# Optimization experiments

Hardware: AMD Instinct MI355X
Metric: run time of the kernel (lower is better)

The kernel has to match this reference:

```python
import jax, jax.numpy as jnp
import numpy as np

NEG_SLOPE = 0.01  # torch nn.LeakyReLU default


def setup_inputs() -> dict:
    key = jax.random.key(0)
    k1, k2, k3, k4 = jax.random.split(key, 4)
    B, N, d = 256, 64, 64
    embeddings = jax.random.normal(k1, (B, N, d), dtype=jnp.float32)
    # nn.Linear(em_dim, em_dim): weight [d, d] (out, in), bias [d]
    w_W = jax.random.normal(k2, (d, d), dtype=jnp.float32) / np.sqrt(d)
    w_b = jax.random.normal(k3, (d,), dtype=jnp.float32) * 0.01
    # nn.Linear(em_dim, 1): weight [1, d] -> stored as [d], bias [1]
    a_W = jax.random.normal(k4, (d,), dtype=jnp.float32) / np.sqrt(d)
    a_b = jnp.zeros((1,), dtype=jnp.float32)
    return {"embeddings": embeddings, "w_W": w_W, "w_b": w_b, "a_W": a_W, "a_b": a_b}


def reference(embeddings, w_W, w_b, a_W, a_b):
    # pairwise elementwise product: value[b,i,j,d] = emb[b,i,d] * emb[b,j,d]
    value = embeddings[:, :, None, :] * embeddings[:, None, :, :]  # [B,N,N,d]
    # small linear d->d (torch Linear: x @ W.T + b)
    qk = jnp.einsum('bijd,ed->bije', value, w_W) + w_b
    qk = jnp.where(qk >= 0, qk, NEG_SLOPE * qk)  # LeakyReLU
    # dropout is identity in eval mode
    logits = jnp.einsum('bijd,d->bij', qk, a_W) + a_b[0]  # linear d->1, squeeze
    alphas = jax.nn.softmax(logits, axis=-1)[..., None]  # [B,N,N,1]
    return alphas, value
```

## Files before the change

### kernel.cpp

```cpp
#include <hip/hip_runtime.h>

typedef __attribute__((ext_vector_type(8))) short short8;
typedef __attribute__((ext_vector_type(4))) float floatx4;

#define NEG_SLOPE 0.01f

__device__ __forceinline__ unsigned bfr(float f) {
    unsigned u = __float_as_uint(f);
    return (u + 0x7FFFu + ((u >> 16) & 1u)) >> 16;
}
__device__ __forceinline__ int pack2(float x, float y) {
    return (int)bfr(x) | (int)(bfr(y) << 16);
}
__device__ __forceinline__ short8 packfrag(float4 a, float4 b) {
    union { int i[4]; short8 s; } u;
    u.i[0] = pack2(a.x, a.y); u.i[1] = pack2(a.z, a.w);
    u.i[2] = pack2(b.x, b.y); u.i[3] = pack2(b.z, b.w);
    return u.s;
}

__global__ __launch_bounds__(256, 4)
void afm_kernel(const float* __restrict__ emb,
                const float* __restrict__ wW,
                const float* __restrict__ wb,
                const float* __restrict__ aW,
                float* __restrict__ aOut,
                float* __restrict__ vOut) {
    __shared__ float slog[4][64];

    const int tid  = threadIdx.x;
    const int lane = tid & 63;
    const int w    = tid >> 6;
    const int lo   = lane & 15;
    const int hi   = lane >> 4;
    const int blk  = blockIdx.x;
    const int b    = blk >> 4;
    const int i    = ((blk & 15) << 2) + w;

    const float* embB   = emb + ((size_t)b << 12);
    const float* ei_row = embB + (i << 6);

    {
        float4 ei = *(const float4*)(ei_row + (lo << 2));
        float* base = vOut + (((size_t)((b << 6) + i)) << 12) + (lane << 2);
        #pragma unroll
        for (int c = 0; c < 16; ++c) {
            float4 ej = *(const float4*)(embB + ((((c << 2) + hi)) << 6) + (lo << 2));
            floatx4 v;
            v[0] = ei.x * ej.x; v[1] = ei.y * ej.y;
            v[2] = ei.z * ej.z; v[3] = ei.w * ej.w;
            __builtin_nontemporal_store(v, (floatx4*)(base + (c << 8)));
        }
    }

    floatx4 acc[4][4];
    #pragma unroll
    for (int jt = 0; jt < 4; ++jt)
        #pragma unroll
        for (int et = 0; et < 4; ++et)
            acc[jt][et] = (floatx4){0.f, 0.f, 0.f, 0.f};

    #pragma unroll
    for (int kt = 0; kt < 2; ++kt) {
        const int d0 = (kt << 5) + (hi << 3);
        float4 ei0 = *(const float4*)(ei_row + d0);
        float4 ei1 = *(const float4*)(ei_row + d0 + 4);
        short8 bfrag[4];
        #pragma unroll
        for (int et = 0; et < 4; ++et) {
            const float* pw = wW + ((((et << 4) + lo)) << 6) + d0;
            float4 w0 = *(const float4*)(pw);
            float4 w1 = *(const float4*)(pw + 4);
            float4 p0, p1;
            p0.x = w0.x * ei0.x; p0.y = w0.y * ei0.y;
            p0.z = w0.z * ei0.z; p0.w = w0.w * ei0.w;
            p1.x = w1.x * ei1.x; p1.y = w1.y * ei1.y;
            p1.z = w1.z * ei1.z; p1.w = w1.w * ei1.w;
            bfrag[et] = packfrag(p0, p1);
        }
        #pragma unroll
        for (int jt = 0; jt < 4; ++jt) {
            const float* pe = embB + ((((jt << 4) + lo)) << 6) + d0;
            float4 a0 = *(const float4*)(pe);
            float4 a1 = *(const float4*)(pe + 4);
            short8 afrag = packfrag(a0, a1);
            #pragma unroll
            for (int et = 0; et < 4; ++et)
                acc[jt][et] = __builtin_amdgcn_mfma_f32_16x16x32_bf16(
                    afrag, bfrag[et], acc[jt][et], 0, 0, 0);
        }
    }

    float wbv[4], awv[4];
    #pragma unroll
    for (int et = 0; et < 4; ++et) {
        wbv[et] = wb[(et << 4) + lo];
        awv[et] = aW[(et << 4) + lo];
    }

    float lg[16];
    #pragma unroll
    for (int jt = 0; jt < 4; ++jt) {
        #pragma unroll
        for (int r = 0; r < 4; ++r) {
            float p = 0.f;
            #pragma unroll
            for (int et = 0; et < 4; ++et) {
                float x = acc[jt][et][r] + wbv[et];
                x = (x >= 0.f) ? x : NEG_SLOPE * x;
                p += awv[et] * x;
            }
            p += __shfl_xor(p, 1);
            p += __shfl_xor(p, 2);
            p += __shfl_xor(p, 4);
            p += __shfl_xor(p, 8);
            lg[jt * 4 + r] = p;
        }
    }

    float m = lg[0];
    #pragma unroll
    for (int k = 1; k < 16; ++k) m = fmaxf(m, lg[k]);
    m = fmaxf(m, __shfl_xor(m, 16));
    m = fmaxf(m, __shfl_xor(m, 32));

    float ex[16];
    float s = 0.f;
    #pragma unroll
    for (int k = 0; k < 16; ++k) { ex[k] = __expf(lg[k] - m); s += ex[k]; }
    s += __shfl_xor(s, 16);
    s += __shfl_xor(s, 32);
    float inv = 1.f / s;

    if (lo == 0) {
        #pragma unroll
        for (int jt = 0; jt < 4; ++jt)
            #pragma unroll
            for (int r = 0; r < 4; ++r)
                slog[w][jt * 16 + hi * 4 + r] = ex[jt * 4 + r] * inv;
    }
    asm volatile("" ::: "memory");
    aOut[(((size_t)((b << 6) + i)) << 6) + lane] = slog[w][lane];
}

extern "C" void kernel_launch(void* const* d_in, const int* in_sizes, int n_in,
                              void* d_out, int out_size, void* d_ws, size_t ws_size,
                              hipStream_t stream) {
    const float* emb = (const float*)d_in[0];
    const float* wW  = (const float*)d_in[1];
    const float* wb  = (const float*)d_in[2];
    const float* aW  = (const float*)d_in[3];
    float* aOut = (float*)d_out;
    float* vOut = aOut + (size_t)256 * 64 * 64;
    afm_kernel<<<4096, 256, 0, stream>>>(emb, wW, wb, aW, aOut, vOut);
}
```

Baseline: 329.8 us.

## Stage batch embeddings in LDS as fp32 and bf16, hoist weight fragments

Each block now loads the 64x64 embedding tile of its batch into shared memory once, keeping an fp32 copy for the value products and a pre-packed bf16 copy for the MFMA A fragments. This replaces the repeated global loads and per-wave bf16 packing. All weight-fragment and bias loads are hoisted to the start so their latency overlaps the staging. The value stores also switch from nontemporal to ordinary stores, which may affect cache pollution for the large output. The change adds a __syncthreads and about 18KB of LDS per block, which may limit occupancy.

```diff
diff --git a/kernel.cpp b/kernel.cpp
--- a/kernel.cpp
+++ b/kernel.cpp
@@ -2,6 +2,7 @@
 
 typedef __attribute__((ext_vector_type(8))) short short8;
 typedef __attribute__((ext_vector_type(4))) float floatx4;
+typedef __attribute__((ext_vector_type(4))) int   intx4;
 
 #define NEG_SLOPE 0.01f
 
@@ -26,6 +27,8 @@
                 const float* __restrict__ aW,
                 float* __restrict__ aOut,
                 float* __restrict__ vOut) {
+    __shared__ __align__(16) float sEf[64][68];
+    __shared__ __align__(16) short sEb[64][72];
     __shared__ float slog[4][64];
 
     const int tid  = threadIdx.x;
@@ -40,16 +43,70 @@
     const float* embB   = emb + ((size_t)b << 12);
     const float* ei_row = embB + (i << 6);
 
+    const int srow = tid >> 2;
+    const int c0   = (tid & 3) << 4;
+    const float* src = embB + (srow << 6) + c0;
+    float4 a0 = *(const float4*)(src);
+    float4 a1 = *(const float4*)(src + 4);
+    float4 a2 = *(const float4*)(src + 8);
+    float4 a3 = *(const float4*)(src + 12);
+
+    float4 eiv = *(const float4*)(ei_row + (lo << 2));
+    float4 ei0[2], ei1[2];
+    #pragma unroll
+    for (int kt = 0; kt < 2; ++kt) {
+        const int d0 = (kt << 5) + (hi << 3);
+        ei0[kt] = *(const float4*)(ei_row + d0);
+        ei1[kt] = *(const float4*)(ei_row + d0 + 4);
+    }
+
+    short8 bfragAll[2][4];
+    #pragma unroll
+    for (int kt = 0; kt < 2; ++kt) {
+        const int d0 = (kt << 5) + (hi << 3);
+        #pragma unroll
+        for (int et = 0; et < 4; ++et) {
+            const float* pw = wW + (((et << 4) + lo) << 6) + d0;
+            float4 w0 = *(const float4*)(pw);
+            float4 w1 = *(const float4*)(pw + 4);
+            float4 p0, p1;
+            p0.x = w0.x * ei0[kt].x; p0.y = w0.y * ei0[kt].y;
+            p0.z = w0.z * ei0[kt].z; p0.w = w0.w * ei0[kt].w;
+            p1.x = w1.x * ei1[kt].x; p1.y = w1.y * ei1[kt].y;
+            p1.z = w1.z * ei1[kt].z; p1.w = w1.w * ei1[kt].w;
+            bfragAll[kt][et] = packfrag(p0, p1);
+        }
+    }
+
+    float wbv[4], awv[4];
+    #pragma unroll
+    for (int et = 0; et < 4; ++et) {
+        wbv[et] = wb[(et << 4) + lo];
+        awv[et] = aW[(et << 4) + lo];
+    }
+
+    *(float4*)&sEf[srow][c0]      = a0;
+    *(float4*)&sEf[srow][c0 + 4]  = a1;
+    *(float4*)&sEf[srow][c0 + 8]  = a2;
+    *(float4*)&sEf[srow][c0 + 12] = a3;
+    intx4 q0, q1;
+    q0[0] = pack2(a0.x, a0.y); q0[1] = pack2(a0.z, a0.w);
+    q0[2] = pack2(a1.x, a1.y); q0[3] = pack2(a1.z, a1.w);
+    q1[0] = pack2(a2.x, a2.y); q1[1] = pack2(a2.z, a2.w);
+    q1[2] = pack2(a3.x, a3.y); q1[3] = pack2(a3.z, a3.w);
+    *(intx4*)&sEb[srow][c0]     = q0;
+    *(intx4*)&sEb[srow][c0 + 8] = q1;
+    __syncthreads();
+
     {
-        float4 ei = *(const float4*)(ei_row + (lo << 2));
         float* base = vOut + (((size_t)((b << 6) + i)) << 12) + (lane << 2);
         #pragma unroll
         for (int c = 0; c < 16; ++c) {
-            float4 ej = *(const float4*)(embB + ((((c << 2) + hi)) << 6) + (lo << 2));
-            floatx4 v;
-            v[0] = ei.x * ej.x; v[1] = ei.y * ej.y;
-            v[2] = ei.z * ej.z; v[3] = ei.w * ej.w;
-            __builtin_nontemporal_store(v, (floatx4*)(base + (c << 8)));
+            float4 ej = *(float4*)&sEf[(c << 2) + hi][lo << 2];
+            float4 v;
+            v.x = eiv.x * ej.x; v.y = eiv.y * ej.y;
+            v.z = eiv.z * ej.z; v.w = eiv.w * ej.w;
+            *(float4*)(base + (c << 8)) = v;
         }
     }
 
@@ -63,39 +120,14 @@
     #pragma unroll
     for (int kt = 0; kt < 2; ++kt) {
         const int d0 = (kt << 5) + (hi << 3);
-        float4 ei0 = *(const float4*)(ei_row + d0);
-        float4 ei1 = *(const float4*)(ei_row + d0 + 4);
-        short8 bfrag[4];
-        #pragma unroll
-        for (int et = 0; et < 4; ++et) {
-            const float* pw = wW + ((((et << 4) + lo)) << 6) + d0;
-            float4 w0 = *(const float4*)(pw);
-            float4 w1 = *(const float4*)(pw + 4);
-            float4 p0, p1;
-            p0.x = w0.x * ei0.x; p0.y = w0.y * ei0.y;
-            p0.z = w0.z * ei0.z; p0.w = w0.w * ei0.w;
-            p1.x = w1.x * ei1.x; p1.y = w1.y * ei1.y;
-            p1.z = w1.z * ei1.z; p1.w = w1.w * ei1.w;
-            bfrag[et] = packfrag(p0, p1);
-        }
         #pragma unroll
         for (int jt = 0; jt < 4; ++jt) {
-            const float* pe = embB + ((((jt << 4) + lo)) << 6) + d0;
-            float4 a0 = *(const float4*)(pe);
-            float4 a1 = *(const float4*)(pe + 4);
-            short8 afrag = packfrag(a0, a1);
+            short8 afrag = *(short8*)&sEb[(jt << 4) + lo][d0];
             #pragma unroll
             for (int et = 0; et < 4; ++et)
                 acc[jt][et] = __builtin_amdgcn_mfma_f32_16x16x32_bf16(
-                    afrag, bfrag[et], acc[jt][et], 0, 0, 0);
+                    afrag, bfragAll[kt][et], acc[jt][et], 0, 0, 0);
         }
-    }
-
-    float wbv[4], awv[4];
-    #pragma unroll
-    for (int et = 0; et < 4; ++et) {
-        wbv[et] = wb[(et << 4) + lo];
-        awv[et] = aW[(et << 4) + lo];
     }
 
     float lg[16];
```

Result: faster. 305.3 us (-7.4%).
